# Kernel tuning notes

Hardware: AMD Instinct MI355X
Metric: run time of the kernel (lower is better)

Reference implementation:

```python
import jax, jax.numpy as jnp
import numpy as np

B, T, C, H, N, FFN = 4, 1024, 2048, 32, 64, 7168
HEAD_DIVISOR = 8.0
EPS = 1e-5


def setup_inputs() -> dict:
    key = jax.random.key(0)
    ks = jax.random.split(key, 30)
    rn = lambda k, s, sc=0.02: jax.random.normal(k, s, jnp.float32) * sc
    ru = lambda k, s: jax.random.uniform(k, s, jnp.float32)
    return {
        "x": jax.random.normal(ks[0], (B, T, C), jnp.float32),
        "att_shift": jax.random.normal(ks[1], (B, C), jnp.float32),
        "wkv_state": jax.random.normal(ks[2], (B, H, N, N), jnp.float32) * 0.1,
        "ffn_shift": jax.random.normal(ks[3], (B, C), jnp.float32),
        "ln1_w": jnp.ones((C,), jnp.float32), "ln1_b": jnp.zeros((C,), jnp.float32),
        "ln2_w": jnp.ones((C,), jnp.float32), "ln2_b": jnp.zeros((C,), jnp.float32),
        "mix_k": ru(ks[4], (C,)), "mix_v": ru(ks[5], (C,)),
        "mix_r": ru(ks[6], (C,)), "mix_g": ru(ks[7], (C,)),
        "Wr": rn(ks[8], (C, C)), "Wk": rn(ks[9], (C, C)), "Wv": rn(ks[10], (C, C)),
        "Wg": rn(ks[11], (C, C)), "Wo": rn(ks[12], (C, C)),
        "time_decay": jax.random.normal(ks[13], (H, N), jnp.float32) * 0.5,
        "time_faaaa": jax.random.normal(ks[14], (H, N), jnp.float32) * 0.1,
        "gn_w": jnp.ones((C,), jnp.float32), "gn_b": jnp.zeros((C,), jnp.float32),
        "cmix_k": ru(ks[15], (C,)), "cmix_r": ru(ks[16], (C,)),
        "Wck": rn(ks[17], (C, FFN)), "Wcr": rn(ks[18], (C, C)), "Wcv": rn(ks[19], (FFN, C)),
    }


def _ln(z, w, b):
    m = z.mean(-1, keepdims=True)
    v = z.var(-1, keepdims=True)
    return (z - m) / jnp.sqrt(v + EPS) * w + b


def _shift(x, shift_state):
    # prepend carried last-token state, drop final position
    return jnp.concatenate([shift_state[:, None, :], x[:, :-1]], axis=1)


def reference(x, att_shift, wkv_state, ffn_shift, ln1_w, ln1_b, ln2_w, ln2_b,
              mix_k, mix_v, mix_r, mix_g, Wr, Wk, Wv, Wg, Wo,
              time_decay, time_faaaa, gn_w, gn_b, cmix_k, cmix_r, Wck, Wcr, Wcv):
    Bb, Tt, Cc = x.shape

    # ---- TimeMix ----
    x1 = _ln(x, ln1_w, ln1_b)
    xx = _shift(x1, att_shift)
    xk = x1 * mix_k + xx * (1 - mix_k)
    xv = x1 * mix_v + xx * (1 - mix_v)
    xr = x1 * mix_r + xx * (1 - mix_r)
    xg = x1 * mix_g + xx * (1 - mix_g)
    r = (xr @ Wr).reshape(Bb, Tt, H, N)
    k = (xk @ Wk).reshape(Bb, Tt, H, N)
    v = (xv @ Wv).reshape(Bb, Tt, H, N)
    g = jax.nn.silu(xg @ Wg)

    w = jnp.exp(-jnp.exp(time_decay))[None, :, :, None]  # [1,H,N,1] decay on k-index
    u = time_faaaa[None, :, :, None]                      # [1,H,N,1] bonus on current token

    def step(S, rkv):  # S: [B,H,N,N] (k-index i, v-index j)
        rr, kk, vv = rkv
        kv = kk[..., :, None] * vv[..., None, :]          # [B,H,N,N]
        y = jnp.einsum('bhi,bhij->bhj', rr, S + u * kv)
        return S * w + kv, y

    rkv = (jnp.moveaxis(r, 1, 0), jnp.moveaxis(k, 1, 0), jnp.moveaxis(v, 1, 0))
    new_wkv, ys = jax.lax.scan(step, wkv_state, rkv)      # ys: [T,B,H,N]
    att = jnp.moveaxis(ys, 0, 1)                          # [B,T,H,N]

    # GroupNorm(n_head groups) on att / head_size_divisor
    z = att / HEAD_DIVISOR
    m = z.mean(-1, keepdims=True)
    var = z.var(-1, keepdims=True)
    z = (z - m) / jnp.sqrt(var + EPS)
    z = z * gn_w.reshape(H, N) + gn_b.reshape(H, N)
    att_out = (z.reshape(Bb, Tt, Cc) * g) @ Wo

    x = x + att_out

    # ---- ChannelMix ----
    x2 = _ln(x, ln2_w, ln2_b)
    xx2 = _shift(x2, ffn_shift)
    xck = x2 * cmix_k + xx2 * (1 - cmix_k)
    xcr = x2 * cmix_r + xx2 * (1 - cmix_r)
    kk = jnp.square(jax.nn.relu(xck @ Wck))
    kv = kk @ Wcv
    ffn_out = jax.nn.sigmoid(xcr @ Wcr) * kv
    x = x + ffn_out

    return x, x1[:, -1], new_wkv, x2[:, -1]
```

## Files before the change

kernel.cpp:

```cpp
#include <hip/hip_runtime.h>
#include <cstdint>
#include <cstddef>

typedef unsigned short u16;
typedef unsigned int u32;
typedef short bf16x8 __attribute__((ext_vector_type(8)));
typedef unsigned short u16x4 __attribute__((ext_vector_type(4)));
typedef unsigned short u16x8 __attribute__((ext_vector_type(8)));
typedef float f32x4 __attribute__((ext_vector_type(4)));

#define DEV __device__ __forceinline__

constexpr int Bb = 4, Tt = 1024, Cc = 2048, Hh = 32, Nd = 64, FF = 7168;
constexpr int BT = Bb * Tt;
constexpr int NCH = 16;

DEV u16 f2bf(float f) {
  union { float f; unsigned u; } un; un.f = f;
  unsigned r = un.u + 0x7FFFu + ((un.u >> 16) & 1u);
  return (u16)(r >> 16);
}
DEV float bf2f(u16 h) {
  union { unsigned u; float f; } un; un.u = ((unsigned)h) << 16;
  return un.f;
}
DEV void gll16(const u16* gp, u16* lp) {
  __builtin_amdgcn_global_load_lds(
      (const __attribute__((address_space(1))) unsigned int*)gp,
      (__attribute__((address_space(3))) unsigned int*)lp,
      16, 0, 0);
}

__global__ void transpose_to_bf16(const float* __restrict__ W, u16* __restrict__ Wt,
                                  int Kk, int Nn) {
  __shared__ float tile[32][33];
  int n0 = blockIdx.x * 32, k0 = blockIdx.y * 32;
  int tx = threadIdx.x & 31, ty = threadIdx.x >> 5;
  #pragma unroll
  for (int r = 0; r < 32; r += 8)
    tile[r + ty][tx] = W[(size_t)(k0 + r + ty) * Nn + n0 + tx];
  __syncthreads();
  #pragma unroll
  for (int r = 0; r < 32; r += 8)
    Wt[(size_t)(n0 + r + ty) * Kk + k0 + tx] = f2bf(tile[tx][r + ty]);
}

DEV void block_ln(const float* __restrict__ src, int tid, float* red,
                  float vals[8], float& mean, float& inv) {
  float s = 0.f, ss = 0.f;
  #pragma unroll
  for (int i = 0; i < 8; i++) {
    float t = src[tid + i * 256];
    vals[i] = t; s += t; ss += t * t;
  }
  #pragma unroll
  for (int m = 1; m < 64; m <<= 1) { s += __shfl_xor(s, m); ss += __shfl_xor(ss, m); }
  int lane = tid & 63, wv = tid >> 6;
  __syncthreads();
  if (lane == 0) { red[wv] = s; red[4 + wv] = ss; }
  __syncthreads();
  s = red[0] + red[1] + red[2] + red[3];
  ss = red[4] + red[5] + red[6] + red[7];
  mean = s * (1.f / Cc);
  float var = ss * (1.f / Cc) - mean * mean;
  inv = rsqrtf(var + 1e-5f);
}

__global__ __launch_bounds__(256)
void ln_mix4(const float* __restrict__ x, const float* __restrict__ shift,
             const float* __restrict__ w, const float* __restrict__ b,
             const float* __restrict__ mk, const float* __restrict__ mv,
             const float* __restrict__ mr, const float* __restrict__ mg,
             u16* __restrict__ xk, u16* __restrict__ xv,
             u16* __restrict__ xr, u16* __restrict__ xg,
             float* __restrict__ last) {
  int row = blockIdx.x;
  int t = row & (Tt - 1), bb = row >> 10;
  int tid = threadIdx.x;
  __shared__ float red[8];
  const float* cur = x + (size_t)row * Cc;
  float cv[8], pv[8], cm, ci, pm = 0.f, pi = 1.f;
  block_ln(cur, tid, red, cv, cm, ci);
  bool t0 = (t == 0);
  const float* prev = t0 ? (shift + (size_t)bb * Cc) : (cur - Cc);
  if (!t0) {
    block_ln(prev, tid, red, pv, pm, pi);
  } else {
    #pragma unroll
    for (int i = 0; i < 8; i++) pv[i] = prev[tid + i * 256];
  }
  size_t o = (size_t)row * Cc;
  bool isLast = (t == Tt - 1);
  #pragma unroll
  for (int i = 0; i < 8; i++) {
    int c = tid + i * 256;
    float xc = (cv[i] - cm) * ci * w[c] + b[c];
    float xp = t0 ? pv[i] : (pv[i] - pm) * pi * w[c] + b[c];
    xk[o + c] = f2bf(xp + mk[c] * (xc - xp));
    xv[o + c] = f2bf(xp + mv[c] * (xc - xp));
    xr[o + c] = f2bf(xp + mr[c] * (xc - xp));
    xg[o + c] = f2bf(xp + mg[c] * (xc - xp));
    if (isLast) last[(size_t)bb * Cc + c] = xc;
  }
}

__global__ __launch_bounds__(256)
void ln_mix2(const float* __restrict__ x, const float* __restrict__ shift,
             const float* __restrict__ w, const float* __restrict__ b,
             const float* __restrict__ ck, const float* __restrict__ cr,
             u16* __restrict__ xck, u16* __restrict__ xcr,
             float* __restrict__ last) {
  int row = blockIdx.x;
  int t = row & (Tt - 1), bb = row >> 10;
  int tid = threadIdx.x;
  __shared__ float red[8];
  const float* cur = x + (size_t)row * Cc;
  float cv[8], pv[8], cm, ci, pm = 0.f, pi = 1.f;
  block_ln(cur, tid, red, cv, cm, ci);
  bool t0 = (t == 0);
  const float* prev = t0 ? (shift + (size_t)bb * Cc) : (cur - Cc);
  if (!t0) {
    block_ln(prev, tid, red, pv, pm, pi);
  } else {
    #pragma unroll
    for (int i = 0; i < 8; i++) pv[i] = prev[tid + i * 256];
  }
  size_t o = (size_t)row * Cc;
  bool isLast = (t == Tt - 1);
  #pragma unroll
  for (int i = 0; i < 8; i++) {
    int c = tid + i * 256;
    float xc = (cv[i] - cm) * ci * w[c] + b[c];
    float xp = t0 ? pv[i] : (pv[i] - pm) * pi * w[c] + b[c];
    xck[o + c] = f2bf(xp + ck[c] * (xc - xp));
    xcr[o + c] = f2bf(xp + cr[c] * (xc - xp));
    if (isLast) last[(size_t)bb * Cc + c] = xc;
  }
}


DEV int swzoff(int row, int off) {
  return (row << 7) +
         (off ^ ((((row >> 1) & 1) << 4) | (((row >> 2) & 1) << 5) | (((row >> 3) & 1) << 6)));
}

DEV void stage_half(const u16* __restrict__ gbase, int ldK, u16* slot, int tid) {
  #pragma unroll
  for (int c2 = 0; c2 < 2; c2++) {
    const int D = c2 * 8192 + tid * 16;
    const int row = D >> 7;
    const int off = (D & 127) ^ ((((row >> 1) & 1) << 4) | (((row >> 2) & 1) << 5) | (((row >> 3) & 1) << 6));
    gll16(gbase + (size_t)row * ldK + (off >> 1), (u16*)((char*)slot + D));
  }
}

template <int EPI>
DEV void g256_core(const u16* __restrict__ A, const u16* __restrict__ Bt,
                   int N, int K,
                   float* __restrict__ Co, u16* __restrict__ Cb,
                   const float* __restrict__ X1, const float* __restrict__ X2,
                   u16 (*lds)[8192], int m0, int n0, int act) {
  const int tid = threadIdx.x;
  const int w = tid >> 6, lane = tid & 63;
  const int l15 = lane & 15, l4 = lane >> 4;
  const int wm = (w & 3) * 64, wn = (w >> 2) * 128;
  const int ahalf = wm >> 7;
  const int arow0 = wm & 127;
  const int bhalf = wn >> 7;
  const int nt = K >> 6;

  const u16* Ag = A + (size_t)m0 * K;
  const u16* Bg = Bt + (size_t)n0 * K;

  f32x4 acc[4][8] = {};
  bf16x8 a[4][2];

  stage_half(Ag, K, lds[0], tid);
  stage_half(Ag + (size_t)128 * K, K, lds[1], tid);
  stage_half(Bg, K, lds[4], tid);
  stage_half(Bg + (size_t)128 * K, K, lds[5], tid);
  if (nt > 1) {
    stage_half(Ag + 64, K, lds[2], tid);
    stage_half(Ag + (size_t)128 * K + 64, K, lds[3], tid);
    asm volatile("s_waitcnt vmcnt(4)" ::: "memory");
  } else {
    asm volatile("s_waitcnt vmcnt(0)" ::: "memory");
  }
  asm volatile("s_barrier" ::: "memory");

  for (int t = 0; t < nt; t++) {
    const int buf = t & 1;
    const char* Aslot = (const char*)lds[buf * 2 + ahalf];
    const char* Bslot = (const char*)lds[4 + buf * 2 + bhalf];

#define G256_PHASE(p)                                                                       \
    {                                                                                       \
      constexpr int nh = (p) >> 1, kh = (p) & 1;                                            \
      if constexpr ((p) < 2) {                                                              \
        _Pragma("unroll")                                                                   \
        for (int mf = 0; mf < 4; mf++) {                                                    \
          const int row = arow0 + mf * 16 + l15;                                            \
          a[mf][kh] = *(const bf16x8*)(Aslot + swzoff(row, kh * 64 + l4 * 16));             \
        }                                                                                   \
      }                                                                                     \
      bf16x8 bfr[4];                                                                        \
      _Pragma("unroll")                                                                     \
      for (int j = 0; j < 4; j++) {                                                         \
        const int row = (nh * 4 + j) * 16 + l15;                                            \
        bfr[j] = *(const bf16x8*)(Bslot + swzoff(row, kh * 64 + l4 * 16));                  \
      }                                                                                     \
      if constexpr ((p) == 0) {                                                             \
        if (t + 1 < nt) stage_half(Bg + (size_t)(t + 1) * 64, K,                            \
                                   lds[4 + (((t + 1) & 1) << 1)], tid);                     \
      } else if constexpr ((p) == 1) {                                                      \
        if (t + 1 < nt) stage_half(Bg + (size_t)128 * K + (size_t)(t + 1) * 64, K,          \
                                   lds[4 + (((t + 1) & 1) << 1) + 1], tid);                 \
      } else if constexpr ((p) == 2) {                                                      \
        if (t + 2 < nt) stage_half(Ag + (size_t)(t + 2) * 64, K, lds[buf << 1], tid);       \
      } else {                                                                              \
        if (t + 2 < nt) stage_half(Ag + (size_t)128 * K + (size_t)(t + 2) * 64, K,          \
                                   lds[(buf << 1) + 1], tid);                               \
      }                                                                                     \
      asm volatile("s_barrier" ::: "memory");                                               \
      __builtin_amdgcn_s_setprio(1);                                                       \
      _Pragma("unroll")                                                                     \
      for (int mf = 0; mf < 4; mf++)                                                        \
        _Pragma("unroll")                                                                   \
        for (int j = 0; j < 4; j++)                                                         \
          acc[mf][nh * 4 + j] = __builtin_amdgcn_mfma_f32_16x16x32_bf16(                    \
              a[mf][kh], bfr[j], acc[mf][nh * 4 + j], 0, 0, 0);                             \
      __builtin_amdgcn_s_setprio(0);                                                       \
      if constexpr ((p) == 3) {                                                             \
        if (t + 2 < nt) asm volatile("s_waitcnt vmcnt(4)" ::: "memory");                    \
        else            asm volatile("s_waitcnt vmcnt(0)" ::: "memory");                    \
      }                                                                                     \
      asm volatile("s_barrier" ::: "memory");                                               \
    }

    G256_PHASE(0)
    G256_PHASE(1)
    G256_PHASE(2)
    G256_PHASE(3)
#undef G256_PHASE
  }

  #pragma unroll
  for (int mf = 0; mf < 4; mf++) {
    #pragma unroll
    for (int reg = 0; reg < 4; reg++) {
      const int gr = m0 + wm + mf * 16 + l4 * 4 + reg;
      const size_t ro = (size_t)gr * N;
      #pragma unroll
      for (int nf = 0; nf < 8; nf++) {
        const int gc = n0 + wn + nf * 16 + l15;
        float val = acc[mf][nf][reg];
        if constexpr (EPI == 0) {
          Co[ro + gc] = val;
        } else if constexpr (EPI == 1) {
          if (act) val = val / (1.f + __expf(-val));
          Cb[ro + gc] = f2bf(val);
        } else if constexpr (EPI == 3) {
          float tr = fmaxf(val, 0.f);
          Cb[ro + gc] = f2bf(tr * tr);
        } else if constexpr (EPI == 4) {
          Co[ro + gc] = X1[ro + gc] + val;
        } else {
          float s = 1.f / (1.f + __expf(-val));
          Co[ro + gc] = fmaf(s, X2[ro + gc], X1[ro + gc]);
        }
      }
    }
  }
}

template <int EPI>
__global__ __launch_bounds__(512, 2)
void gemm256(const u16* __restrict__ A, const u16* __restrict__ Bt,
             int N, int K,
             float* __restrict__ Co, u16* __restrict__ Cb,
             const float* __restrict__ X1, const float* __restrict__ X2) {
  __shared__ __align__(16) u16 lds[8][8192];
  g256_core<EPI>(A, Bt, N, K, Co, Cb, X1, X2, lds, blockIdx.y * 256, blockIdx.x * 256, 0);
}

__global__ __launch_bounds__(512, 2)
void gemm256_proj(const u16* __restrict__ A0, const u16* __restrict__ A1,
                  const u16* __restrict__ A2, const u16* __restrict__ A3,
                  const u16* __restrict__ B0, const u16* __restrict__ B1,
                  const u16* __restrict__ B2, const u16* __restrict__ B3,
                  u16* __restrict__ C0, u16* __restrict__ C1,
                  u16* __restrict__ C2, u16* __restrict__ C3) {
  __shared__ __align__(16) u16 lds[8][8192];
  const int z = blockIdx.z;
  const u16* A = (z == 0) ? A0 : (z == 1) ? A1 : (z == 2) ? A2 : A3;
  const u16* Bt = (z == 0) ? B0 : (z == 1) ? B1 : (z == 2) ? B2 : B3;
  u16* Cb = (z == 0) ? C0 : (z == 1) ? C1 : (z == 2) ? C2 : C3;
  g256_core<1>(A, Bt, Cc, Cc, nullptr, Cb, nullptr, nullptr, lds,
               blockIdx.y * 256, blockIdx.x * 256, z == 3);
}

__global__ __launch_bounds__(256)
void wkv_pre(const u16* __restrict__ rg, const u16* __restrict__ kg,
             const u16* __restrict__ vg, const float* __restrict__ td,
             const float* __restrict__ tf,
             float* __restrict__ Yb, float* __restrict__ Db,
             u16* __restrict__ Rtb) {
  __shared__ float Pt[64][68];
  __shared__ float uL[64];
  __shared__ u16 rB[64 * 72];
  __shared__ u16 kB[64 * 72];
  __shared__ u16 Rh[64 * 72];
  __shared__ u16 KhX[96 * 72];
  __shared__ u16 vA[64 * 72];
  __shared__ u16 Vt[64 * 72];

  const int tid = threadIdx.x, bid = blockIdx.x;
  const int bh = bid >> 4, c = bid & 15;
  const int b = bh >> 5, h = bh & 31;
  const int lane = tid & 63, w = tid >> 6;

  {
    int i = tid & 63;
    float d = __expf(td[h * 64 + i]);
    float c1 = -1.4426950408889634f * d;
    int e0 = (tid >> 6) * 16;
    #pragma unroll
    for (int e = 0; e < 16; e++) Pt[e0 + e][i] = exp2f(c1 * (float)(e0 + e));
    if (tid < 64) uL[tid] = tf[h * 64 + tid];
  }
  __syncthreads();

  const int row = tid >> 2, col0 = (tid & 3) * 16;
  const int tl = row & 15;
  {
    size_t gro = ((size_t)b * Tt + c * 64 + row) * Cc + h * 64 + col0;
    u16x8 rv0 = *(const u16x8*)(rg + gro);
    u16x8 rv1 = *(const u16x8*)(rg + gro + 8);
    u16x8 kv0 = *(const u16x8*)(kg + gro);
    u16x8 kv1 = *(const u16x8*)(kg + gro + 8);
    u16x8 vv0 = *(const u16x8*)(vg + gro);
    u16x8 vv1 = *(const u16x8*)(vg + gro + 8);
    *(u16x8*)&rB[row * 72 + col0] = rv0; *(u16x8*)&rB[row * 72 + col0 + 8] = rv1;
    *(u16x8*)&kB[row * 72 + col0] = kv0; *(u16x8*)&kB[row * 72 + col0 + 8] = kv1;
    *(u16x8*)&vA[row * 72 + col0] = vv0; *(u16x8*)&vA[row * 72 + col0 + 8] = vv1;
    float rf[16], kf[16];
    #pragma unroll
    for (int e = 0; e < 8; e++) { rf[e] = bf2f(rv0[e]); rf[8 + e] = bf2f(rv1[e]); }
    #pragma unroll
    for (int e = 0; e < 8; e++) { kf[e] = bf2f(kv0[e]); kf[8 + e] = bf2f(kv1[e]); }
    u16x8 o0, o1, t0_, t1_;
    #pragma unroll
    for (int e = 0; e < 8; e++) {
      o0[e] = f2bf(rf[e] * Pt[tl][col0 + e]);
      o1[e] = f2bf(rf[8 + e] * Pt[tl][col0 + 8 + e]);
      t0_[e] = f2bf(rf[e] * Pt[row][col0 + e]);
      t1_[e] = f2bf(rf[8 + e] * Pt[row][col0 + 8 + e]);
    }
    *(u16x8*)&Rh[row * 72 + col0] = o0; *(u16x8*)&Rh[row * 72 + col0 + 8] = o1;
    u16* rtp = Rtb + (size_t)bid * 4096 + row * 64 + col0;
    *(u16x8*)rtp = t0_; *(u16x8*)(rtp + 8) = t1_;
    if (row < 48) {
      u16x8 a0, a1;
      #pragma unroll
      for (int e = 0; e < 8; e++) {
        a0[e] = f2bf(kf[e] * Pt[15 - tl][col0 + e]);
        a1[e] = f2bf(kf[8 + e] * Pt[15 - tl][col0 + 8 + e]);
      }
      *(u16x8*)&KhX[row * 72 + col0] = a0; *(u16x8*)&KhX[row * 72 + col0 + 8] = a1;
    }
    if (row < 32) {
      u16x8 a0, a1;
      #pragma unroll
      for (int e = 0; e < 8; e++) {
        a0[e] = f2bf(kf[e] * Pt[31 - tl][col0 + e]);
        a1[e] = f2bf(kf[8 + e] * Pt[31 - tl][col0 + 8 + e]);
      }
      *(u16x8*)&KhX[(48 + row) * 72 + col0] = a0; *(u16x8*)&KhX[(48 + row) * 72 + col0 + 8] = a1;
    }
    if (row < 16) {
      u16x8 a0, a1;
      #pragma unroll
      for (int e = 0; e < 8; e++) {
        a0[e] = f2bf(kf[e] * Pt[47 - tl][col0 + e]);
        a1[e] = f2bf(kf[8 + e] * Pt[47 - tl][col0 + 8 + e]);
      }
      *(u16x8*)&KhX[(80 + row) * 72 + col0] = a0; *(u16x8*)&KhX[(80 + row) * 72 + col0 + 8] = a1;
    }
  }
  __syncthreads();

  {
    const int jj = tid & 63, s0 = (tid >> 6) * 16;
    #pragma unroll
    for (int ds = 0; ds < 16; ds += 2) {
      u32 pk = ((u32)vA[(s0 + ds + 1) * 72 + jj] << 16) | vA[(s0 + ds) * 72 + jj];
      *(u32*)&Vt[jj * 72 + s0 + ds] = pk;
    }
  }
  __syncthreads();

  u16* aB = vA;
  {
    const int pr[6] = {1, 2, 3, 2, 3, 3};
    const int qr[6] = {0, 1, 2, 0, 1, 0};
    const int dr[6] = {0, 0, 0, 1, 1, 2};
    const int lr = lane & 15, kq = lane >> 4;
    for (int pi = w; pi < 6; pi += 4) {
      const int p = pr[pi], q = qr[pi], d = dr[pi];
      const int kbase = (d == 0) ? q * 16 : (d == 1) ? 48 + q * 16 : 80 + q * 16;
      f32x4 aacc = {};
      #pragma unroll
      for (int kf2 = 0; kf2 < 2; kf2++) {
        bf16x8 af = *(const bf16x8*)&Rh[(p * 16 + lr) * 72 + kf2 * 32 + kq * 8];
        bf16x8 bf_ = *(const bf16x8*)&KhX[(kbase + lr) * 72 + kf2 * 32 + kq * 8];
        aacc = __builtin_amdgcn_mfma_f32_16x16x32_bf16(af, bf_, aacc, 0, 0, 0);
      }
      #pragma unroll
      for (int reg = 0; reg < 4; reg++) {
        aB[(p * 16 + kq * 4 + reg) * 72 + q * 16 + lr] = f2bf(aacc[reg]);
        aB[(q * 16 + kq * 4 + reg) * 72 + p * 16 + lr] = 0;
      }
    }
    for (int e = lane; e < 256; e += 64) {
      const int tl2 = e >> 4, sl = e & 15;
      float a = 0.f;
      if (sl <= tl2) {
        const u16* rp = &rB[(w * 16 + tl2) * 72];
        const u16* kp = &kB[(w * 16 + sl) * 72];
        const float* pp = (sl == tl2) ? uL : &Pt[tl2 - 1 - sl][0];
        #pragma unroll
        for (int i0 = 0; i0 < 64; i0 += 4) {
          u16x4 ra = *(const u16x4*)(rp + i0);
          u16x4 ka = *(const u16x4*)(kp + i0);
          f32x4 pa = *(const f32x4*)(pp + i0);
          #pragma unroll
          for (int di = 0; di < 4; di++)
            a = fmaf(bf2f(ra[di]) * bf2f(ka[di]), pa[di], a);
        }
      }
      aB[(w * 16 + tl2) * 72 + w * 16 + sl] = f2bf(a);
    }
  }
  __syncthreads();

  u16* Ktt = KhX;
  {
    const int ii = tid & 63, s0 = (tid >> 6) * 16;
    #pragma unroll
    for (int ds = 0; ds < 16; ds += 2) {
      float v0 = bf2f(kB[(s0 + ds) * 72 + ii]) * Pt[63 - (s0 + ds)][ii];
      float v1 = bf2f(kB[(s0 + ds + 1) * 72 + ii]) * Pt[63 - (s0 + ds + 1)][ii];
      u32 pk = ((u32)f2bf(v1) << 16) | f2bf(v0);
      *(u32*)&Ktt[ii * 72 + s0 + ds] = pk;
    }
  }
  __syncthreads();

  const int lr = lane & 15, kq = lane >> 4;
  {
    f32x4 yac[4] = {};
    #pragma unroll
    for (int kf2 = 0; kf2 < 2; kf2++) {
      bf16x8 af = *(const bf16x8*)&aB[(w * 16 + lr) * 72 + kf2 * 32 + kq * 8];
      #pragma unroll
      for (int nf = 0; nf < 4; nf++) {
        bf16x8 bf_ = *(const bf16x8*)&Vt[(nf * 16 + lr) * 72 + kf2 * 32 + kq * 8];
        yac[nf] = __builtin_amdgcn_mfma_f32_16x16x32_bf16(af, bf_, yac[nf], 0, 0, 0);
      }
    }
    float* Yp = Yb + (size_t)bid * 4096;
    #pragma unroll
    for (int nf = 0; nf < 4; nf++)
      #pragma unroll
      for (int reg = 0; reg < 4; reg++)
        Yp[(w * 16 + kq * 4 + reg) * 64 + nf * 16 + lr] = yac[nf][reg];

    f32x4 dac[4] = {};
    #pragma unroll
    for (int kf2 = 0; kf2 < 2; kf2++) {
      bf16x8 af = *(const bf16x8*)&Ktt[(w * 16 + lr) * 72 + kf2 * 32 + kq * 8];
      #pragma unroll
      for (int nf = 0; nf < 4; nf++) {
        bf16x8 bf_ = *(const bf16x8*)&Vt[(nf * 16 + lr) * 72 + kf2 * 32 + kq * 8];
        dac[nf] = __builtin_amdgcn_mfma_f32_16x16x32_bf16(af, bf_, dac[nf], 0, 0, 0);
      }
    }
    float* Dp = Db + (size_t)bid * 4096;
    #pragma unroll
    for (int nf = 0; nf < 4; nf++)
      #pragma unroll
      for (int reg = 0; reg < 4; reg++)
        Dp[(w * 16 + kq * 4 + reg) * 64 + nf * 16 + lr] = dac[nf][reg];
  }
}

__global__ __launch_bounds__(256)
void wkv_scan(const float* __restrict__ s0g, const float* __restrict__ td,
              const float* __restrict__ Db, u16* __restrict__ Sbb,
              float* __restrict__ sout) {
  const int bh = blockIdx.x, h = bh & 31;
  const int tid = threadIdx.x;
  const int i = tid >> 2, j0 = (tid & 3) * 16;
  float d = __expf(td[h * 64 + i]);
  float w64 = exp2f(-1.4426950408889634f * d * 64.f);
  f32x4 S[4];
  const float* sp = s0g + ((size_t)bh * 64 + i) * 64 + j0;
  #pragma unroll
  for (int q = 0; q < 4; q++) S[q] = *(const f32x4*)(sp + q * 4);
  for (int c = 0; c < NCH; c++) {
    u16* op = Sbb + ((size_t)(bh * 16 + c)) * 4096 + i * 64 + j0;
    u16x8 o0, o1;
    #pragma unroll
    for (int e = 0; e < 4; e++) { o0[e] = f2bf(S[0][e]); o0[4 + e] = f2bf(S[1][e]);
                                  o1[e] = f2bf(S[2][e]); o1[4 + e] = f2bf(S[3][e]); }
    *(u16x8*)op = o0; *(u16x8*)(op + 8) = o1;
    const float* dp = Db + ((size_t)(bh * 16 + c)) * 4096 + i * 64 + j0;
    #pragma unroll
    for (int q = 0; q < 4; q++) {
      f32x4 dv = *(const f32x4*)(dp + q * 4);
      #pragma unroll
      for (int e = 0; e < 4; e++) S[q][e] = fmaf(w64, S[q][e], dv[e]);
    }
  }
  float* fo = sout + ((size_t)bh * 64 + i) * 64 + j0;
  #pragma unroll
  for (int q = 0; q < 4; q++) *(f32x4*)(fo + q * 4) = S[q];
}

__global__ __launch_bounds__(256)
void wkv_post(const u16* __restrict__ Rtb, const u16* __restrict__ Sbb,
              const float* __restrict__ Yb, const u16* __restrict__ g,
              const float* __restrict__ gnw, const float* __restrict__ gnb,
              u16* __restrict__ xo) {
  __shared__ u16 Rt[64 * 72];
  __shared__ u16 St[64 * 72];
  __shared__ u16 xoL[64 * 72];
  const int tid = threadIdx.x, bid = blockIdx.x;
  const int bh = bid >> 4, c = bid & 15;
  const int b = bh >> 5, h = bh & 31;
  const int lane = tid & 63, w = tid >> 6;
  const int row = tid >> 2, col0 = (tid & 3) * 16;

  {
    const u16* rp = Rtb + (size_t)bid * 4096 + row * 64 + col0;
    u16x8 a0 = *(const u16x8*)rp, a1 = *(const u16x8*)(rp + 8);
    *(u16x8*)&Rt[row * 72 + col0] = a0; *(u16x8*)&Rt[row * 72 + col0 + 8] = a1;
  }
  {
    const u16* sp = Sbb + ((size_t)(bh * 16 + c)) * 4096 + row * 64 + col0;
    u16x8 s0 = *(const u16x8*)sp, s1 = *(const u16x8*)(sp + 8);
    #pragma unroll
    for (int e = 0; e < 8; e++) {
      St[(col0 + e) * 72 + row] = s0[e];
      St[(col0 + 8 + e) * 72 + row] = s1[e];
    }
  }
  const int lr = lane & 15, kq = lane >> 4;
  f32x4 acc[4];
  {
    const float* Yp = Yb + (size_t)bid * 4096;
    #pragma unroll
    for (int nf = 0; nf < 4; nf++)
      #pragma unroll
      for (int reg = 0; reg < 4; reg++)
        acc[nf][reg] = Yp[(w * 16 + kq * 4 + reg) * 64 + nf * 16 + lr];
  }
  __syncthreads();
  #pragma unroll
  for (int kf2 = 0; kf2 < 2; kf2++) {
    bf16x8 af = *(const bf16x8*)&Rt[(w * 16 + lr) * 72 + kf2 * 32 + kq * 8];
    #pragma unroll
    for (int nf = 0; nf < 4; nf++) {
      bf16x8 bf_ = *(const bf16x8*)&St[(nf * 16 + lr) * 72 + kf2 * 32 + kq * 8];
      acc[nf] = __builtin_amdgcn_mfma_f32_16x16x32_bf16(af, bf_, acc[nf], 0, 0, 0);
    }
  }
  #pragma unroll
  for (int reg = 0; reg < 4; reg++) {
    float s = 0.f, ss = 0.f;
    #pragma unroll
    for (int nf = 0; nf < 4; nf++) {
      float z = acc[nf][reg] * 0.125f;
      s += z; ss += z * z;
    }
    #pragma unroll
    for (int m = 1; m < 16; m <<= 1) { s += __shfl_xor(s, m); ss += __shfl_xor(ss, m); }
    float mean = s * (1.f / 64.f);
    float var = ss * (1.f / 64.f) - mean * mean;
    float inv = rsqrtf(var + 1e-5f);
    const int tau = w * 16 + kq * 4 + reg;
    #pragma unroll
    for (int nf = 0; nf < 4; nf++) {
      const int col = nf * 16 + lr;
      float z = acc[nf][reg] * 0.125f;
      float zn = (z - mean) * inv * gnw[h * 64 + col] + gnb[h * 64 + col];
      float gv = bf2f(g[((size_t)b * Tt + c * 64 + tau) * Cc + h * 64 + col]);
      xoL[tau * 72 + col] = f2bf(zn * gv);
    }
  }
  __syncthreads();
  {
    u16x8 o0 = *(const u16x8*)&xoL[row * 72 + col0];
    u16x8 o1 = *(const u16x8*)&xoL[row * 72 + col0 + 8];
    u16* xop = xo + ((size_t)b * Tt + c * 64 + row) * Cc + h * 64 + col0;
    *(u16x8*)xop = o0; *(u16x8*)(xop + 8) = o1;
  }
}

extern "C" void kernel_launch(void* const* d_in, const int* in_sizes, int n_in,
                              void* d_out, int out_size, void* d_ws, size_t ws_size,
                              hipStream_t stream) {
  const float* x         = (const float*)d_in[0];
  const float* att_shift = (const float*)d_in[1];
  const float* wkv0      = (const float*)d_in[2];
  const float* ffn_shift = (const float*)d_in[3];
  const float* ln1w = (const float*)d_in[4];
  const float* ln1b = (const float*)d_in[5];
  const float* ln2w = (const float*)d_in[6];
  const float* ln2b = (const float*)d_in[7];
  const float* mixk = (const float*)d_in[8];
  const float* mixv = (const float*)d_in[9];
  const float* mixr = (const float*)d_in[10];
  const float* mixg = (const float*)d_in[11];
  const float* Wr = (const float*)d_in[12];
  const float* Wk = (const float*)d_in[13];
  const float* Wv = (const float*)d_in[14];
  const float* Wg = (const float*)d_in[15];
  const float* Wo = (const float*)d_in[16];
  const float* td = (const float*)d_in[17];
  const float* tf = (const float*)d_in[18];
  const float* gnw = (const float*)d_in[19];
  const float* gnb = (const float*)d_in[20];
  const float* cmk = (const float*)d_in[21];
  const float* cmr = (const float*)d_in[22];
  const float* Wck = (const float*)d_in[23];
  const float* Wcr = (const float*)d_in[24];
  const float* Wcv = (const float*)d_in[25];

  constexpr size_t SZ_CC = (size_t)Cc * Cc * 2;
  constexpr size_t SZ_CF = (size_t)Cc * FF * 2;
  constexpr size_t SZ_AB = (size_t)BT * Cc * 2;
  constexpr size_t O_W   = 0;
  constexpr size_t O_R1  = 6 * SZ_CC + 2 * SZ_CF;
  constexpr size_t R1_SZ = 4 * SZ_AB;
  constexpr size_t O_R2  = O_R1 + R1_SZ;
  constexpr size_t R2_SZ = 3 * SZ_AB;
  constexpr size_t O_R3  = O_R2 + R2_SZ;
  constexpr size_t WS_NEED = O_R3 + SZ_AB;

  if (ws_size < WS_NEED) return;

  char* ws = (char*)d_ws;
  u16* WrT  = (u16*)(ws + O_W);
  u16* WkT  = (u16*)(ws + O_W + 1 * SZ_CC);
  u16* WvT  = (u16*)(ws + O_W + 2 * SZ_CC);
  u16* WgT  = (u16*)(ws + O_W + 3 * SZ_CC);
  u16* WoT  = (u16*)(ws + O_W + 4 * SZ_CC);
  u16* WcrT = (u16*)(ws + O_W + 5 * SZ_CC);
  u16* WckT = (u16*)(ws + O_W + 6 * SZ_CC);
  u16* WcvT = (u16*)(ws + O_W + 6 * SZ_CC + SZ_CF);

  u16*   xk  = (u16*)(ws + O_R1);
  u16*   xv  = (u16*)(ws + O_R1 + SZ_AB);
  u16*   xr  = (u16*)(ws + O_R1 + 2 * SZ_AB);
  u16*   xg  = (u16*)(ws + O_R1 + 3 * SZ_AB);
  float* Yb  = (float*)(ws + O_R1);
  u16*   Rtb = (u16*)(ws + O_R1 + 2 * SZ_AB);
  u16*   Sbb = (u16*)(ws + O_R1 + 3 * SZ_AB);
  u16*   kk  = (u16*)(ws + O_R1);
  u16*   rb  = (u16*)(ws + O_R2);
  u16*   kb  = (u16*)(ws + O_R2 + SZ_AB);
  u16*   vb  = (u16*)(ws + O_R2 + 2 * SZ_AB);
  u16*   xo  = (u16*)(ws + O_R2);
  u16*   xck = (u16*)(ws + O_R2 + SZ_AB);
  u16*   xcr = (u16*)(ws + O_R2 + 2 * SZ_AB);
  float* kv  = (float*)(ws + O_R2);
  u16*   gbuf = (u16*)(ws + O_R3);

  float* out      = (float*)d_out;
  float* x1_last  = out + (size_t)BT * Cc;
  float* wkv_out  = x1_last + (size_t)Bb * Cc;
  float* x2_last  = wkv_out + (size_t)Bb * Hh * Nd * Nd;
  float* Db       = out;

  transpose_to_bf16<<<dim3(64, 64), 256, 0, stream>>>(Wr, WrT, Cc, Cc);
  transpose_to_bf16<<<dim3(64, 64), 256, 0, stream>>>(Wk, WkT, Cc, Cc);
  transpose_to_bf16<<<dim3(64, 64), 256, 0, stream>>>(Wv, WvT, Cc, Cc);
  transpose_to_bf16<<<dim3(64, 64), 256, 0, stream>>>(Wg, WgT, Cc, Cc);
  transpose_to_bf16<<<dim3(64, 64), 256, 0, stream>>>(Wo, WoT, Cc, Cc);
  transpose_to_bf16<<<dim3(64, 64), 256, 0, stream>>>(Wcr, WcrT, Cc, Cc);
  transpose_to_bf16<<<dim3(224, 64), 256, 0, stream>>>(Wck, WckT, Cc, FF);
  transpose_to_bf16<<<dim3(64, 224), 256, 0, stream>>>(Wcv, WcvT, FF, Cc);

  ln_mix4<<<BT, 256, 0, stream>>>(x, att_shift, ln1w, ln1b,
                                  mixk, mixv, mixr, mixg, xk, xv, xr, xg, x1_last);
  gemm256_proj<<<dim3(8, 16, 4), 512, 0, stream>>>(xr, xk, xv, xg,
                                                   WrT, WkT, WvT, WgT,
                                                   rb, kb, vb, gbuf);
  wkv_pre<<<Bb * Hh * NCH, 256, 0, stream>>>(rb, kb, vb, td, tf, Yb, Db, Rtb);
  wkv_scan<<<Bb * Hh, 256, 0, stream>>>(wkv0, td, Db, Sbb, wkv_out);
  wkv_post<<<Bb * Hh * NCH, 256, 0, stream>>>(Rtb, Sbb, Yb, gbuf, gnw, gnb, xo);
  gemm256<4><<<dim3(8, 16), 512, 0, stream>>>(xo, WoT, Cc, Cc, out, nullptr, x, nullptr);
  ln_mix2<<<BT, 256, 0, stream>>>(out, ffn_shift, ln2w, ln2b, cmk, cmr, xck, xcr, x2_last);
  gemm256<3><<<dim3(28, 16), 512, 0, stream>>>(xck, WckT, FF, Cc, nullptr, kk, nullptr, nullptr);
  gemm256<0><<<dim3(8, 16), 512, 0, stream>>>(kk, WcvT, Cc, FF, kv, nullptr, nullptr, nullptr);
  gemm256<5><<<dim3(8, 16), 512, 0, stream>>>(xcr, WcrT, Cc, Cc, out, nullptr, out, kv);

  (void)in_sizes; (void)n_in; (void)out_size;
}
```

Before: 809.4 us.

## Use 256x128 GEMM tiles for N=2048 GEMMs and batch square weight transposes

Adds an NB-templated GEMM core so the Wo, Wcv and Wcr GEMMs (N=2048) run with 256x128 tiles, doubling the grid from 128 to 256 blocks to fill more of the GPU's compute units. It also merges six separate square weight-transpose launches into one kernel indexed by blockIdx.z to cut launch overhead. The narrower tiles lower per-block arithmetic intensity and increase A-tile reloads from memory.

```diff
diff --git a/kernel.cpp b/kernel.cpp
--- a/kernel.cpp
+++ b/kernel.cpp
@@ -31,18 +31,38 @@
       16, 0, 0);
 }
 
+DEV void transp_body(const float* __restrict__ W, u16* __restrict__ Wt,
+                     int Kk, int Nn, float (*tile)[33]) {
+  int n0 = blockIdx.x * 32, k0 = blockIdx.y * 32;
+  int tx = threadIdx.x & 31, ty = threadIdx.x >> 5;
+  #pragma unroll
+  for (int r = 0; r < 32; r += 8)
+    tile[r + ty][tx] = W[(size_t)(k0 + r + ty) * Nn + n0 + tx];
+  __syncthreads();
+  #pragma unroll
+  for (int r = 0; r < 32; r += 8)
+    Wt[(size_t)(n0 + r + ty) * Kk + k0 + tx] = f2bf(tile[tx][r + ty]);
+}
+
 __global__ void transpose_to_bf16(const float* __restrict__ W, u16* __restrict__ Wt,
                                   int Kk, int Nn) {
   __shared__ float tile[32][33];
-  int n0 = blockIdx.x * 32, k0 = blockIdx.y * 32;
-  int tx = threadIdx.x & 31, ty = threadIdx.x >> 5;
-  #pragma unroll
-  for (int r = 0; r < 32; r += 8)
-    tile[r + ty][tx] = W[(size_t)(k0 + r + ty) * Nn + n0 + tx];
-  __syncthreads();
-  #pragma unroll
-  for (int r = 0; r < 32; r += 8)
-    Wt[(size_t)(n0 + r + ty) * Kk + k0 + tx] = f2bf(tile[tx][r + ty]);
+  transp_body(W, Wt, Kk, Nn, tile);
+}
+
+__global__ void transpose6_cc(const float* __restrict__ W0, const float* __restrict__ W1,
+                              const float* __restrict__ W2, const float* __restrict__ W3,
+                              const float* __restrict__ W4, const float* __restrict__ W5,
+                              u16* __restrict__ T0, u16* __restrict__ T1,
+                              u16* __restrict__ T2, u16* __restrict__ T3,
+                              u16* __restrict__ T4, u16* __restrict__ T5) {
+  __shared__ float tile[32][33];
+  const int z = blockIdx.z;
+  const float* W = (z == 0) ? W0 : (z == 1) ? W1 : (z == 2) ? W2 :
+                   (z == 3) ? W3 : (z == 4) ? W4 : W5;
+  u16* T = (z == 0) ? T0 : (z == 1) ? T1 : (z == 2) ? T2 :
+           (z == 3) ? T3 : (z == 4) ? T4 : T5;
+  transp_body(W, T, Cc, Cc, tile);
 }
 
 DEV void block_ln(const float* __restrict__ src, int tid, float* red,
@@ -154,7 +174,7 @@
   }
 }
 
-template <int EPI>
+template <int EPI, int NB>
 DEV void g256_core(const u16* __restrict__ A, const u16* __restrict__ Bt,
                    int N, int K,
                    float* __restrict__ Co, u16* __restrict__ Cb,
@@ -163,22 +183,23 @@
   const int tid = threadIdx.x;
   const int w = tid >> 6, lane = tid & 63;
   const int l15 = lane & 15, l4 = lane >> 4;
-  const int wm = (w & 3) * 64, wn = (w >> 2) * 128;
+  const int wm = (w & 3) * 64;
+  const int wn = (w >> 2) * (NB * 64);
   const int ahalf = wm >> 7;
   const int arow0 = wm & 127;
-  const int bhalf = wn >> 7;
+  const int bhalf = (NB == 2) ? (w >> 2) : 0;
   const int nt = K >> 6;
 
   const u16* Ag = A + (size_t)m0 * K;
   const u16* Bg = Bt + (size_t)n0 * K;
 
-  f32x4 acc[4][8] = {};
+  f32x4 acc[4][NB * 4] = {};
   bf16x8 a[4][2];
 
   stage_half(Ag, K, lds[0], tid);
   stage_half(Ag + (size_t)128 * K, K, lds[1], tid);
   stage_half(Bg, K, lds[4], tid);
-  stage_half(Bg + (size_t)128 * K, K, lds[5], tid);
+  if constexpr (NB == 2) stage_half(Bg + (size_t)128 * K, K, lds[5], tid);
   if (nt > 1) {
     stage_half(Ag + 64, K, lds[2], tid);
     stage_half(Ag + (size_t)128 * K + 64, K, lds[3], tid);
@@ -191,7 +212,7 @@
   for (int t = 0; t < nt; t++) {
     const int buf = t & 1;
     const char* Aslot = (const char*)lds[buf * 2 + ahalf];
-    const char* Bslot = (const char*)lds[4 + buf * 2 + bhalf];
+    const char* Bslot = (const char*)lds[4 + buf * NB + bhalf];
 
 #define G256_PHASE(p)                                                                       \
     {                                                                                       \
@@ -203,18 +224,20 @@
           a[mf][kh] = *(const bf16x8*)(Aslot + swzoff(row, kh * 64 + l4 * 16));             \
         }                                                                                   \
       }                                                                                     \
-      bf16x8 bfr[4];                                                                        \
+      bf16x8 bfr[2 * NB];                                                                   \
       _Pragma("unroll")                                                                     \
-      for (int j = 0; j < 4; j++) {                                                         \
-        const int row = (nh * 4 + j) * 16 + l15;                                            \
+      for (int j = 0; j < 2 * NB; j++) {                                                    \
+        const int row = (NB == 2 ? 0 : wn) + (nh * 2 * NB + j) * 16 + l15;                  \
         bfr[j] = *(const bf16x8*)(Bslot + swzoff(row, kh * 64 + l4 * 16));                  \
       }                                                                                     \
       if constexpr ((p) == 0) {                                                             \
         if (t + 1 < nt) stage_half(Bg + (size_t)(t + 1) * 64, K,                            \
-                                   lds[4 + (((t + 1) & 1) << 1)], tid);                     \
+                                   lds[4 + ((t + 1) & 1) * NB], tid);                       \
       } else if constexpr ((p) == 1) {                                                      \
-        if (t + 1 < nt) stage_half(Bg + (size_t)128 * K + (size_t)(t + 1) * 64, K,          \
-                                   lds[4 + (((t + 1) & 1) << 1) + 1], tid);                 \
+        if constexpr (NB == 2) {                                                            \
+          if (t + 1 < nt) stage_half(Bg + (size_t)128 * K + (size_t)(t + 1) * 64, K,        \
+                                     lds[4 + ((t + 1) & 1) * NB + 1], tid);                 \
+        }                                                                                   \
       } else if constexpr ((p) == 2) {                                                      \
         if (t + 2 < nt) stage_half(Ag + (size_t)(t + 2) * 64, K, lds[buf << 1], tid);       \
       } else {                                                                              \
@@ -226,9 +249,9 @@
       _Pragma("unroll")                                                                     \
       for (int mf = 0; mf < 4; mf++)                                                        \
         _Pragma("unroll")                                                                   \
-        for (int j = 0; j < 4; j++)                                                         \
-          acc[mf][nh * 4 + j] = __builtin_amdgcn_mfma_f32_16x16x32_bf16(                    \
-              a[mf][kh], bfr[j], acc[mf][nh * 4 + j], 0, 0, 0);                             \
+        for (int j = 0; j < 2 * NB; j++)                                                    \
+          acc[mf][nh * 2 * NB + j] = __builtin_amdgcn_mfma_f32_16x16x32_bf16(               \
+              a[mf][kh], bfr[j], acc[mf][nh * 2 * NB + j], 0, 0, 0);                        \
       __builtin_amdgcn_s_setprio(0);                                                       \
       if constexpr ((p) == 3) {                                                             \
         if (t + 2 < nt) asm volatile("s_waitcnt vmcnt(4)" ::: "memory");                    \
@@ -251,7 +274,7 @@
       const int gr = m0 + wm + mf * 16 + l4 * 4 + reg;
       const size_t ro = (size_t)gr * N;
       #pragma unroll
-      for (int nf = 0; nf < 8; nf++) {
+      for (int nf = 0; nf < NB * 4; nf++) {
         const int gc = n0 + wn + nf * 16 + l15;
         float val = acc[mf][nf][reg];
         if constexpr (EPI == 0) {
@@ -280,7 +303,17 @@
              float* __restrict__ Co, u16* __restrict__ Cb,
              const float* __restrict__ X1, const float* __restrict__ X2) {
   __shared__ __align__(16) u16 lds[8][8192];
-  g256_core<EPI>(A, Bt, N, K, Co, Cb, X1, X2, lds, blockIdx.y * 256, blockIdx.x * 256, 0);
+  g256_core<EPI, 2>(A, Bt, N, K, Co, Cb, X1, X2, lds, blockIdx.y * 256, blockIdx.x * 256, 0);
+}
+
+template <int EPI>
+__global__ __launch_bounds__(512, 2)
+void gemm128n(const u16* __restrict__ A, const u16* __restrict__ Bt,
+              int N, int K,
+              float* __restrict__ Co, u16* __restrict__ Cb,
+              const float* __restrict__ X1, const float* __restrict__ X2) {
+  __shared__ __align__(16) u16 lds[6][8192];
+  g256_core<EPI, 1>(A, Bt, N, K, Co, Cb, X1, X2, lds, blockIdx.y * 256, blockIdx.x * 128, 0);
 }
 
 __global__ __launch_bounds__(512, 2)
@@ -295,8 +328,8 @@
   const u16* A = (z == 0) ? A0 : (z == 1) ? A1 : (z == 2) ? A2 : A3;
   const u16* Bt = (z == 0) ? B0 : (z == 1) ? B1 : (z == 2) ? B2 : B3;
   u16* Cb = (z == 0) ? C0 : (z == 1) ? C1 : (z == 2) ? C2 : C3;
-  g256_core<1>(A, Bt, Cc, Cc, nullptr, Cb, nullptr, nullptr, lds,
-               blockIdx.y * 256, blockIdx.x * 256, z == 3);
+  g256_core<1, 2>(A, Bt, Cc, Cc, nullptr, Cb, nullptr, nullptr, lds,
+                  blockIdx.y * 256, blockIdx.x * 256, z == 3);
 }
 
 __global__ __launch_bounds__(256)
@@ -683,12 +716,8 @@
   float* x2_last  = wkv_out + (size_t)Bb * Hh * Nd * Nd;
   float* Db       = out;
 
-  transpose_to_bf16<<<dim3(64, 64), 256, 0, stream>>>(Wr, WrT, Cc, Cc);
-  transpose_to_bf16<<<dim3(64, 64), 256, 0, stream>>>(Wk, WkT, Cc, Cc);
-  transpose_to_bf16<<<dim3(64, 64), 256, 0, stream>>>(Wv, WvT, Cc, Cc);
-  transpose_to_bf16<<<dim3(64, 64), 256, 0, stream>>>(Wg, WgT, Cc, Cc);
-  transpose_to_bf16<<<dim3(64, 64), 256, 0, stream>>>(Wo, WoT, Cc, Cc);
-  transpose_to_bf16<<<dim3(64, 64), 256, 0, stream>>>(Wcr, WcrT, Cc, Cc);
+  transpose6_cc<<<dim3(64, 64, 6), 256, 0, stream>>>(Wr, Wk, Wv, Wg, Wo, Wcr,
+                                                     WrT, WkT, WvT, WgT, WoT, WcrT);
   transpose_to_bf16<<<dim3(224, 64), 256, 0, stream>>>(Wck, WckT, Cc, FF);
   transpose_to_bf16<<<dim3(64, 224), 256, 0, stream>>>(Wcv, WcvT, FF, Cc);
 
@@ -700,11 +729,11 @@
   wkv_pre<<<Bb * Hh * NCH, 256, 0, stream>>>(rb, kb, vb, td, tf, Yb, Db, Rtb);
   wkv_scan<<<Bb * Hh, 256, 0, stream>>>(wkv0, td, Db, Sbb, wkv_out);
   wkv_post<<<Bb * Hh * NCH, 256, 0, stream>>>(Rtb, Sbb, Yb, gbuf, gnw, gnb, xo);
-  gemm256<4><<<dim3(8, 16), 512, 0, stream>>>(xo, WoT, Cc, Cc, out, nullptr, x, nullptr);
+  gemm128n<4><<<dim3(16, 16), 512, 0, stream>>>(xo, WoT, Cc, Cc, out, nullptr, x, nullptr);
   ln_mix2<<<BT, 256, 0, stream>>>(out, ffn_shift, ln2w, ln2b, cmk, cmr, xck, xcr, x2_last);
   gemm256<3><<<dim3(28, 16), 512, 0, stream>>>(xck, WckT, FF, Cc, nullptr, kk, nullptr, nullptr);
-  gemm256<0><<<dim3(8, 16), 512, 0, stream>>>(kk, WcvT, Cc, FF, kv, nullptr, nullptr, nullptr);
-  gemm256<5><<<dim3(8, 16), 512, 0, stream>>>(xcr, WcrT, Cc, Cc, out, nullptr, out, kv);
+  gemm128n<0><<<dim3(16, 16), 512, 0, stream>>>(kk, WcvT, Cc, FF, kv, nullptr, nullptr, nullptr);
+  gemm128n<5><<<dim3(16, 16), 512, 0, stream>>>(xcr, WcrT, Cc, Cc, out, nullptr, out, kv);
 
   (void)in_sizes; (void)n_in; (void)out_size;
 }
```

Measured after the change: 735.3 us. -9.2%, faster.
